# Kernel optimization log

Measured on AMD Instinct MI355X. Metric: run time of the kernel, lower is better.

The kernel has to match this reference:

```python
import jax, jax.numpy as jnp
import numpy as np

B, S, HID = 1, 2048, 4096
H, KH, D = 32, 8, 128          # query heads, kv heads, head_dim
ROT = 64                       # rotary_dim = head_dim * partial_rotary_factor (0.5)
THETA = 10000.0
EPS = 1e-5
SCALE = D ** -0.5
NEG = -1e30


def setup_inputs() -> dict:
    key = jax.random.key(0)
    ks = jax.random.split(key, 7)
    return {
        "hidden_states": jax.random.normal(ks[0], (B, S, HID), jnp.float32),
        "Wq": jax.random.normal(ks[1], (H * D, HID), jnp.float32) * 0.02,
        "Wk": jax.random.normal(ks[2], (KH * D, HID), jnp.float32) * 0.02,
        "Wv": jax.random.normal(ks[3], (KH * D, HID), jnp.float32) * 0.02,
        "Wo": jax.random.normal(ks[4], (H * D, HID), jnp.float32).T.reshape(HID, H * D) * 0.02,
        "q_norm_w": jax.random.uniform(ks[5], (D,), jnp.float32),
        "k_norm_w": jax.random.uniform(ks[6], (D,), jnp.float32),
        "position_ids": jnp.arange(S, dtype=jnp.int32)[None, :],
    }


def rms_norm(x, w):
    # per-head RMSNorm in fp32, scale by (weight + 1)
    xf = x.astype(jnp.float32)
    var = jnp.mean(xf * xf, axis=-1, keepdims=True)
    return (xf * jax.lax.rsqrt(var + EPS) * (w.astype(jnp.float32) + 1.0)).astype(x.dtype)


def rope_cos_sin(position_ids):
    inv_freq = 1.0 / (THETA ** (jnp.arange(0, ROT, 2, dtype=jnp.float32) / ROT))
    freqs = position_ids.astype(jnp.float32)[..., None] * inv_freq  # [B,S,ROT/2]
    emb = jnp.concatenate([freqs, freqs], axis=-1)                  # [B,S,ROT]
    return jnp.cos(emb)[:, None], jnp.sin(emb)[:, None]             # [B,1,S,ROT]


def rotate_half(x):
    x1, x2 = jnp.split(x, 2, axis=-1)
    return jnp.concatenate([-x2, x1], axis=-1)


def apply_partial_rope(x, cos, sin):
    x_rot, x_pass = x[..., :ROT], x[..., ROT:]
    x_rot = x_rot * cos + rotate_half(x_rot) * sin
    return jnp.concatenate([x_rot, x_pass], axis=-1)


def reference(hidden_states, Wq, Wk, Wv, Wo, q_norm_w, k_norm_w, position_ids):
    # projections -> [B, heads, S, D]
    q = (hidden_states @ Wq.T).reshape(B, S, H, D).transpose(0, 2, 1, 3)
    k = (hidden_states @ Wk.T).reshape(B, S, KH, D).transpose(0, 2, 1, 3)
    v = (hidden_states @ Wv.T).reshape(B, S, KH, D).transpose(0, 2, 1, 3)

    q = rms_norm(q, q_norm_w)
    k = rms_norm(k, k_norm_w)

    cos, sin = rope_cos_sin(position_ids)
    q = apply_partial_rope(q, cos, sin)
    k = apply_partial_rope(k, cos, sin)

    # repeat kv heads (GQA) -> [B, H, S, D]
    rep = H // KH
    k = jnp.broadcast_to(k[:, :, None], (B, KH, rep, S, D)).reshape(B, H, S, D)
    v = jnp.broadcast_to(v[:, :, None], (B, KH, rep, S, D)).reshape(B, H, S, D)

    scores = jnp.einsum("bhqd,bhkd->bhqk", q, k) * SCALE
    causal = jnp.tril(jnp.ones((S, S), bool))
    scores = jnp.where(causal, scores, NEG)
    attn = jax.nn.softmax(scores, axis=-1)
    out = jnp.einsum("bhqk,bhkd->bhqd", attn, v)        # [B,H,S,D]
    out = out.transpose(0, 2, 1, 3).reshape(B, S, H * D)
    return out @ Wo.T                                    # [B,S,HID]
```

## Files before the change

kernel.cpp:

```cpp
#include <hip/hip_runtime.h>
#include <hip/hip_bf16.h>

#define AS1 __attribute__((address_space(1)))
#define AS3 __attribute__((address_space(3)))

typedef __attribute__((ext_vector_type(8))) short short8;
typedef __attribute__((ext_vector_type(4))) short short4v;
typedef __attribute__((ext_vector_type(4))) float f32x4;

constexpr int S_ = 2048;
constexpr int HID_ = 4096;
constexpr int NH = 32;
constexpr int NKH = 8;
constexpr float EPS_ = 1e-5f;
constexpr float SCALE_ = 0.08838834764831845f;

__device__ __forceinline__ short f2bf(float f) {
  __hip_bfloat16 h = __float2bfloat16(f);
  return *reinterpret_cast<short*>(&h);
}

__global__ __launch_bounds__(256) void cast_bf16_kernel(const float4* __restrict__ src,
                                                        short4v* __restrict__ dst, int n4) {
  int i = blockIdx.x * 256 + threadIdx.x;
  if (i >= n4) return;
  float4 v = src[i];
  short4v o;
  o[0] = f2bf(v.x); o[1] = f2bf(v.y); o[2] = f2bf(v.z); o[3] = f2bf(v.w);
  dst[i] = o;
}

template <int G>
__global__ __launch_bounds__(512, 2) void gemm8_bt(const short* __restrict__ A,
                                                   const short* __restrict__ B,
                                                   float* __restrict__ C,
                                                   int M, int N, int K) {
  constexpr int BN = G * 64;
  constexpr int BUFSZ = 32768 + G * 8192;
  constexpr int GH = (G + 1) / 2;
  extern __shared__ __align__(16) char smem[];
  const int t = threadIdx.x, w = t >> 6, lane = t & 63;
  const int nbx = N / BN;
  int wg = blockIdx.x;
  const int cpx = gridDim.x >> 3;
  wg = (wg & 7) * cpx + (wg >> 3);
  const int by = wg / nbx, bx = wg % nbx;
  const long m0 = (long)by * 256, n0 = (long)bx * BN;
  const int wr = w >> 2, wc = w & 3;
  const int l15 = lane & 15, l4 = lane >> 4;
  const int NT = K >> 6;

  f32x4 acc[8][G];
#pragma unroll
  for (int f = 0; f < 8; ++f)
#pragma unroll
    for (int g = 0; g < G; ++g) acc[f][g] = (f32x4){0.f, 0.f, 0.f, 0.f};

  const int srow = w * 8 + (lane >> 3);
  const int schunk = lane & 7;

  auto STAGE = [&](int tile, int unit) {
    int tb = tile & (NT - 1);
    long k0 = (long)tb << 6;
    char* base = smem + (tb & 1) * BUFSZ;
    if (unit < 2) {
#pragma unroll
      for (int j = 0; j < 2; ++j) {
        int row = unit * 128 + j * 64 + srow;
        int ch = schunk ^ (row & 7);
        __builtin_amdgcn_global_load_lds(
            (const AS1 void*)(A + (m0 + row) * K + k0 + ch * 8),
            (AS3 void*)(base + unit * 16384 + j * 8192 + w * 1024 + lane * 16), 16, 0, 0);
      }
    } else {
      int bj = unit - 2;
      int row = bj * 64 + srow;
      int ch = schunk ^ (row & 7);
      __builtin_amdgcn_global_load_lds(
          (const AS1 void*)(B + (n0 + row) * K + k0 + ch * 8),
          (AS3 void*)(base + 32768 + bj * 8192 + w * 1024 + lane * 16), 16, 0, 0);
    }
  };
  auto LDA = [&](int buf, int f, int s) -> short8 {
    int ra = wr * 128 + f * 16 + l15;
    int byte = ra * 128 + (((s << 2) + l4) ^ (ra & 7)) * 16;
    return *(const short8*)(smem + buf * BUFSZ + byte);
  };
  auto LDB = [&](int buf, int g, int s) -> short8 {
    int rb = wc * (G * 16) + g * 16 + l15;
    int byte = 32768 + rb * 128 + (((s << 2) + l4) ^ (rb & 7)) * 16;
    return *(const short8*)(smem + buf * BUFSZ + byte);
  };

#pragma unroll
  for (int u = 0; u < 2 + G; ++u) STAGE(0, u);
  STAGE(1, 0);
  asm volatile("s_waitcnt vmcnt(2)" ::: "memory");
  asm volatile("s_barrier" ::: "memory");

  short8 af[4][2], bf2[G][2];
  for (int tt = 0; tt < NT; ++tt) {
    const int buf = tt & 1;
#pragma unroll
    for (int f = 0; f < 4; ++f) { af[f][0] = LDA(buf, f, 0); af[f][1] = LDA(buf, f, 1); }
#pragma unroll
    for (int g = 0; g < GH; ++g) { bf2[g][0] = LDB(buf, g, 0); bf2[g][1] = LDB(buf, g, 1); }
    STAGE(tt + 1, 1);
    asm volatile("s_barrier" ::: "memory");
    __builtin_amdgcn_s_setprio(1);
#pragma unroll
    for (int f = 0; f < 4; ++f)
#pragma unroll
      for (int g = 0; g < GH; ++g) {
        acc[f][g] = __builtin_amdgcn_mfma_f32_16x16x32_bf16(af[f][0], bf2[g][0], acc[f][g], 0, 0, 0);
        acc[f][g] = __builtin_amdgcn_mfma_f32_16x16x32_bf16(af[f][1], bf2[g][1], acc[f][g], 0, 0, 0);
      }
    __builtin_amdgcn_s_setprio(0);
    asm volatile("s_barrier" ::: "memory");
#pragma unroll
    for (int g = GH; g < G; ++g) { bf2[g][0] = LDB(buf, g, 0); bf2[g][1] = LDB(buf, g, 1); }
#pragma unroll
    for (int u = 2; u < G + 1; ++u) STAGE(tt + 1, u);
    asm volatile("s_barrier" ::: "memory");
    __builtin_amdgcn_s_setprio(1);
#pragma unroll
    for (int f = 0; f < 4; ++f)
#pragma unroll
      for (int g = GH; g < G; ++g) {
        acc[f][g] = __builtin_amdgcn_mfma_f32_16x16x32_bf16(af[f][0], bf2[g][0], acc[f][g], 0, 0, 0);
        acc[f][g] = __builtin_amdgcn_mfma_f32_16x16x32_bf16(af[f][1], bf2[g][1], acc[f][g], 0, 0, 0);
      }
    __builtin_amdgcn_s_setprio(0);
    asm volatile("s_barrier" ::: "memory");
#pragma unroll
    for (int f = 0; f < 4; ++f) { af[f][0] = LDA(buf, 4 + f, 0); af[f][1] = LDA(buf, 4 + f, 1); }
    STAGE(tt + 1, G + 1);
    asm volatile("s_barrier" ::: "memory");
    __builtin_amdgcn_s_setprio(1);
#pragma unroll
    for (int f = 0; f < 4; ++f)
#pragma unroll
      for (int g = 0; g < GH; ++g) {
        acc[4 + f][g] = __builtin_amdgcn_mfma_f32_16x16x32_bf16(af[f][0], bf2[g][0], acc[4 + f][g], 0, 0, 0);
        acc[4 + f][g] = __builtin_amdgcn_mfma_f32_16x16x32_bf16(af[f][1], bf2[g][1], acc[4 + f][g], 0, 0, 0);
      }
    __builtin_amdgcn_s_setprio(0);
    asm volatile("s_barrier" ::: "memory");
    STAGE(tt + 2, 0);
    asm volatile("s_barrier" ::: "memory");
    __builtin_amdgcn_s_setprio(1);
#pragma unroll
    for (int f = 0; f < 4; ++f)
#pragma unroll
      for (int g = GH; g < G; ++g) {
        acc[4 + f][g] = __builtin_amdgcn_mfma_f32_16x16x32_bf16(af[f][0], bf2[g][0], acc[4 + f][g], 0, 0, 0);
        acc[4 + f][g] = __builtin_amdgcn_mfma_f32_16x16x32_bf16(af[f][1], bf2[g][1], acc[4 + f][g], 0, 0, 0);
      }
    __builtin_amdgcn_s_setprio(0);
    asm volatile("s_waitcnt vmcnt(2)" ::: "memory");
    asm volatile("s_barrier" ::: "memory");
  }
#pragma unroll
  for (int f = 0; f < 8; ++f)
#pragma unroll
    for (int g = 0; g < G; ++g)
#pragma unroll
      for (int r = 0; r < 4; ++r) {
        long m = m0 + wr * 128 + f * 16 + l4 * 4 + r;
        long n = n0 + wc * (G * 16) + g * 16 + l15;
        C[m * N + n] = acc[f][g][r];
      }
}

__global__ __launch_bounds__(256) void normrope_kernel(const float* __restrict__ QKV,
    const int* __restrict__ pos_ids, const float* __restrict__ qw,
    const float* __restrict__ kw,
    short* __restrict__ Qn, short* __restrict__ Kn) {
  const int lane = threadIdx.x & 63;
  const long row = (long)blockIdx.x * 4 + (threadIdx.x >> 6);
  const long NQ = (long)S_ * NH;
  const float* src;
  short* dst;
  const float* wv;
  int s;
  float scl = 1.f;
  if (row < NQ) {
    s = (int)(row >> 5); int h = (int)(row & 31);
    src = QKV + (long)s * 6144 + h * 128;
    dst = Qn + ((long)h * S_ + s) * 128;
    wv = qw; scl = SCALE_;
  } else {
    long r2 = row - NQ; s = (int)(r2 >> 3); int kh = (int)(r2 & 7);
    src = QKV + (long)s * 6144 + 4096 + kh * 128;
    dst = Kn + ((long)kh * S_ + s) * 128;
    wv = kw;
  }
  float x0 = src[lane], x1 = src[lane + 64];
  float ss = x0 * x0 + x1 * x1;
#pragma unroll
  for (int m = 1; m < 64; m <<= 1) ss += __shfl_xor(ss, m);
  float inv = rsqrtf(ss * (1.f / 128.f) + EPS_);
  x0 = x0 * inv * (wv[lane] + 1.f);
  x1 = x1 * inv * (wv[lane + 64] + 1.f);
  int pos = pos_ids[s];
  int i = lane & 31;
  float invf = expf(-logf(10000.f) * ((float)(2 * i) / 64.f));
  float f = (float)pos * invf;
  float c = cosf(f), sn = sinf(f);
  float p = __shfl_xor(x0, 32);
  x0 = (lane < 32) ? (x0 * c - p * sn) : (x0 * c + p * sn);
  dst[lane] = f2bf(x0 * scl);
  dst[lane + 64] = f2bf(x1 * scl);
}

__global__ __launch_bounds__(256) void vtrans_kernel(const float* __restrict__ QKV,
                                                     short* __restrict__ Vt) {
  __shared__ __align__(16) float lt[64][68];
  const int t = threadIdx.x;
  const int s0 = blockIdx.x * 64, d0 = blockIdx.y * 64, kh = blockIdx.z;
  const float* src = QKV + (long)s0 * 6144 + 5120 + kh * 128 + d0;
#pragma unroll
  for (int i = 0; i < 4; ++i) {
    int idx = t + i * 256;
    int r = idx >> 4, c4 = (idx & 15) * 4;
    float4 v = *(const float4*)(src + (long)r * 6144 + c4);
    *(float4*)&lt[r][c4] = v;
  }
  __syncthreads();
  int d = t >> 2, seg = (t & 3) * 16;
  short* dst = Vt + ((long)kh * 128 + d0 + d) * S_ + s0 + seg;
  short8 a, b2;
#pragma unroll
  for (int j = 0; j < 8; ++j) a[j] = f2bf(lt[seg + j][d]);
#pragma unroll
  for (int j = 0; j < 8; ++j) b2[j] = f2bf(lt[seg + 8 + j][d]);
  *(short8*)dst = a;
  *(short8*)(dst + 8) = b2;
}

__global__ __launch_bounds__(512, 2) void attn_kernel(const short* __restrict__ Qn,
    const short* __restrict__ Kn, const short* __restrict__ Vt,
    short* __restrict__ O) {
  __shared__ __align__(16) short Ks[64 * 128];
  __shared__ __align__(16) short Vs[128 * 64];
  __shared__ __align__(16) short Ps[8][16 * 64];
  const int t = threadIdx.x, w = t >> 6, lane = t & 63;
  const int b = blockIdx.x;
  const int h = b & 31, qt = 15 - (b >> 5);
  const int kh = h >> 2;
  const int q0 = qt * 128;
  const int l15 = lane & 15, lk = (lane >> 4) * 8;

  short8 qf[4];
  {
    const short* Qh = Qn + ((long)h * S_ + q0 + w * 16) * 128;
#pragma unroll
    for (int ks = 0; ks < 4; ++ks)
      qf[ks] = *(const short8*)(Qh + l15 * 128 + ks * 32 + lk);
  }
  f32x4 o[8];
#pragma unroll
  for (int nf = 0; nf < 8; ++nf) o[nf] = (f32x4){0.f, 0.f, 0.f, 0.f};
  float mrun[4], lrun[4];
#pragma unroll
  for (int r = 0; r < 4; ++r) { mrun[r] = -1e30f; lrun[r] = 0.f; }

  const short* Khp = Kn + (long)kh * S_ * 128;
  const short* Vtp = Vt + (long)kh * 128 * S_;

  const int krr = w * 8 + (lane >> 4);
  const int kc = lane & 15;
  const int vdd = w * 16 + (lane >> 3);
  const int vc = lane & 7;
  char* pw = (char*)Ps[w];
  const int mrow = (lane >> 4) * 4;

  for (int kv0 = 0; kv0 < q0 + 128; kv0 += 64) {
#pragma unroll
    for (int j = 0; j < 2; ++j) {
      int rr = krr + j * 4;
      __builtin_amdgcn_global_load_lds(
          (const AS1 void*)(Khp + (long)(kv0 + rr) * 128 + ((kc ^ (rr & 7)) * 8)),
          (AS3 void*)(Ks + (w * 8 + j * 4) * 128 + lane * 8), 16, 0, 0);
    }
#pragma unroll
    for (int j = 0; j < 2; ++j) {
      int d = vdd + j * 8;
      __builtin_amdgcn_global_load_lds(
          (const AS1 void*)(Vtp + (long)d * S_ + kv0 + ((vc ^ (d & 7)) * 8)),
          (AS3 void*)(Vs + (w * 16 + j * 8) * 64 + lane * 8), 16, 0, 0);
    }
    __syncthreads();

    const bool active = (kv0 <= q0 + w * 16 + 15);
    if (active) {
      f32x4 sc[4];
#pragma unroll
      for (int ni = 0; ni < 4; ++ni) sc[ni] = (f32x4){0.f, 0.f, 0.f, 0.f};
#pragma unroll
      for (int ks = 0; ks < 4; ++ks)
#pragma unroll
        for (int ni = 0; ni < 4; ++ni) {
          int row = ni * 16 + l15;
          int bb = row * 256 + (ks * 32 + lk) * 2; bb ^= (row & 7) << 4;
          short8 kf = *(const short8*)((const char*)Ks + bb);
          sc[ni] = __builtin_amdgcn_mfma_f32_16x16x32_bf16(qf[ks], kf, sc[ni], 0, 0, 0);
        }
      if (kv0 + 64 > q0 + w * 16) {
#pragma unroll
        for (int ni = 0; ni < 4; ++ni)
#pragma unroll
          for (int r = 0; r < 4; ++r) {
            int qm = q0 + w * 16 + mrow + r;
            int kcol = kv0 + ni * 16 + l15;
            if (kcol > qm) sc[ni][r] = -1e30f;
          }
      }
      short pb[4][4];
#pragma unroll
      for (int r = 0; r < 4; ++r) {
        float mx = fmaxf(fmaxf(sc[0][r], sc[1][r]), fmaxf(sc[2][r], sc[3][r]));
        mx = fmaxf(mx, __shfl_xor(mx, 1));
        mx = fmaxf(mx, __shfl_xor(mx, 2));
        mx = fmaxf(mx, __shfl_xor(mx, 4));
        mx = fmaxf(mx, __shfl_xor(mx, 8));
        float mnew = fmaxf(mrun[r], mx);
        float scale = expf(mrun[r] - mnew);
        mrun[r] = mnew;
        float ssum = 0.f;
#pragma unroll
        for (int ni = 0; ni < 4; ++ni) {
          float p = expf(sc[ni][r] - mnew);
          ssum += p;
          pb[ni][r] = f2bf(p);
        }
        ssum += __shfl_xor(ssum, 1);
        ssum += __shfl_xor(ssum, 2);
        ssum += __shfl_xor(ssum, 4);
        ssum += __shfl_xor(ssum, 8);
        lrun[r] = lrun[r] * scale + ssum;
#pragma unroll
        for (int nf = 0; nf < 8; ++nf) o[nf][r] *= scale;
      }
#pragma unroll
      for (int ni = 0; ni < 4; ++ni)
#pragma unroll
        for (int r = 0; r < 4; ++r) {
          int m = mrow + r;
          int bb = m * 128 + (ni * 16 + l15) * 2; bb ^= (m & 7) << 4;
          *(short*)(pw + bb) = pb[ni][r];
        }
#pragma unroll
      for (int ks2 = 0; ks2 < 2; ++ks2) {
        int bp = l15 * 128 + (ks2 * 32 + lk) * 2; bp ^= (l15 & 7) << 4;
        short8 pf = *(const short8*)(pw + bp);
#pragma unroll
        for (int nf = 0; nf < 8; ++nf) {
          int bv = (nf * 16 + l15) * 128 + (ks2 * 32 + lk) * 2; bv ^= (l15 & 7) << 4;
          short8 vf = *(const short8*)((const char*)Vs + bv);
          o[nf] = __builtin_amdgcn_mfma_f32_16x16x32_bf16(pf, vf, o[nf], 0, 0, 0);
        }
      }
    }
    __syncthreads();
  }
#pragma unroll
  for (int r = 0; r < 4; ++r) {
    float invl = 1.f / lrun[r];
    int m = q0 + w * 16 + mrow + r;
#pragma unroll
    for (int nf = 0; nf < 8; ++nf)
      O[(long)m * 4096 + h * 128 + nf * 16 + l15] = f2bf(o[nf][r] * invl);
  }
}

extern "C" void kernel_launch(void* const* d_in, const int* in_sizes, int n_in,
                              void* d_out, int out_size, void* d_ws, size_t ws_size,
                              hipStream_t stream) {
  const float* hidden = (const float*)d_in[0];
  const float* Wq = (const float*)d_in[1];
  const float* Wk = (const float*)d_in[2];
  const float* Wv = (const float*)d_in[3];
  const float* Wo = (const float*)d_in[4];
  const float* qw = (const float*)d_in[5];
  const float* kw = (const float*)d_in[6];
  const int* pos = (const int*)d_in[7];
  float* out = (float*)d_out;

  char* ws = (char*)d_ws;
  short* hid_bf  = (short*)(ws + 0);
  short* Wqkv_bf = (short*)(ws + 16777216L);
  short* Wo_bf   = (short*)(ws + 67108864L);
  float* QKVf    = (float*)(ws + 100663296L);
  short* Qn      = (short*)(ws + 150994944L);
  short* Kn      = (short*)(ws + 167772160L);
  short* Vt      = (short*)(ws + 171966464L);
  short* AO      = hid_bf;

  (void)hipFuncSetAttribute((const void*)gemm8_bt<3>,
                            hipFuncAttributeMaxDynamicSharedMemorySize, 114688);
  (void)hipFuncSetAttribute((const void*)gemm8_bt<2>,
                            hipFuncAttributeMaxDynamicSharedMemorySize, 98304);

  auto cast = [&](const float* s_, short* d_, long n) {
    int n4 = (int)(n / 4);
    cast_bf16_kernel<<<(n4 + 255) / 256, 256, 0, stream>>>((const float4*)s_, (short4v*)d_, n4);
  };
  cast(hidden, hid_bf, (long)S_ * HID_);
  cast(Wq, Wqkv_bf, (long)4096 * 4096);
  cast(Wk, Wqkv_bf + (long)4096 * 4096, (long)1024 * 4096);
  cast(Wv, Wqkv_bf + (long)5120 * 4096, (long)1024 * 4096);
  cast(Wo, Wo_bf, (long)4096 * 4096);

  gemm8_bt<3><<<dim3(256), 512, 114688, stream>>>(hid_bf, Wqkv_bf, QKVf, S_, 6144, HID_);

  normrope_kernel<<<(S_ * (NH + NKH)) / 4, 256, 0, stream>>>(QKVf, pos, qw, kw, Qn, Kn);
  vtrans_kernel<<<dim3(S_ / 64, 2, NKH), 256, 0, stream>>>(QKVf, Vt);
  attn_kernel<<<dim3(512), 512, 0, stream>>>(Qn, Kn, Vt, AO);

  gemm8_bt<2><<<dim3(256), 512, 98304, stream>>>(AO, Wo_bf, out, S_, HID_, HID_);
}
```

Baseline: 524.4 us.

## Double-buffer attention KV tiles, widen per-wave Q rows, fuse casts, use exp2

The attention kernel now runs 4 waves that each own 32 query rows, which doubles K/V fragment reuse per wave. It double-buffers K/V tiles in dynamic LDS so the next tile's global-to-LDS load overlaps compute. The softmax scale is folded with log2(e) so exp2f can replace expf. The five cast launches are merged into one kernel, and the GEMM block-index decode is simplified. In exchange the kernel uses more LDS and registers, and the GEMM index change hardcodes 8 row blocks.

```diff
diff --git a/kernel.cpp b/kernel.cpp
--- a/kernel.cpp
+++ b/kernel.cpp
@@ -14,20 +14,32 @@
 constexpr int NKH = 8;
 constexpr float EPS_ = 1e-5f;
 constexpr float SCALE_ = 0.08838834764831845f;
+constexpr float SCL2E_ = 0.12751879524622712f;
 
 __device__ __forceinline__ short f2bf(float f) {
   __hip_bfloat16 h = __float2bfloat16(f);
   return *reinterpret_cast<short*>(&h);
 }
 
-__global__ __launch_bounds__(256) void cast_bf16_kernel(const float4* __restrict__ src,
-                                                        short4v* __restrict__ dst, int n4) {
-  int i = blockIdx.x * 256 + threadIdx.x;
-  if (i >= n4) return;
-  float4 v = src[i];
-  short4v o;
-  o[0] = f2bf(v.x); o[1] = f2bf(v.y); o[2] = f2bf(v.z); o[3] = f2bf(v.w);
-  dst[i] = o;
+__global__ __launch_bounds__(256) void cast_all_kernel(
+    const float4* __restrict__ h, const float4* __restrict__ wq,
+    const float4* __restrict__ wk, const float4* __restrict__ wv,
+    const float4* __restrict__ wo,
+    short4v* __restrict__ hd, short4v* __restrict__ wqkvd,
+    short4v* __restrict__ wod) {
+  long i = (long)blockIdx.x * 256 + threadIdx.x;
+  const float4* s;
+  short4v* d;
+  long o;
+  if (i < 2097152L)        { s = h;  d = hd;              o = i; }
+  else if (i < 6291456L)   { s = wq; d = wqkvd;           o = i - 2097152L; }
+  else if (i < 7340032L)   { s = wk; d = wqkvd + 4194304L; o = i - 6291456L; }
+  else if (i < 8388608L)   { s = wv; d = wqkvd + 5242880L; o = i - 7340032L; }
+  else                     { s = wo; d = wod;             o = i - 8388608L; }
+  float4 v = s[o];
+  short4v r;
+  r[0] = f2bf(v.x); r[1] = f2bf(v.y); r[2] = f2bf(v.z); r[3] = f2bf(v.w);
+  d[o] = r;
 }
 
 template <int G>
@@ -40,11 +52,10 @@
   constexpr int GH = (G + 1) / 2;
   extern __shared__ __align__(16) char smem[];
   const int t = threadIdx.x, w = t >> 6, lane = t & 63;
-  const int nbx = N / BN;
   int wg = blockIdx.x;
   const int cpx = gridDim.x >> 3;
   wg = (wg & 7) * cpx + (wg >> 3);
-  const int by = wg / nbx, bx = wg % nbx;
+  const int by = wg & 7, bx = wg >> 3;
   const long m0 = (long)by * 256, n0 = (long)bx * BN;
   const int wr = w >> 2, wc = w & 3;
   const int l15 = lane & 15, l4 = lane >> 4;
@@ -188,7 +199,7 @@
     s = (int)(row >> 5); int h = (int)(row & 31);
     src = QKV + (long)s * 6144 + h * 128;
     dst = Qn + ((long)h * S_ + s) * 128;
-    wv = qw; scl = SCALE_;
+    wv = qw; scl = SCL2E_;
   } else {
     long r2 = row - NQ; s = (int)(r2 >> 3); int kh = (int)(r2 & 7);
     src = QKV + (long)s * 6144 + 4096 + kh * 128;
@@ -238,140 +249,165 @@
   *(short8*)(dst + 8) = b2;
 }
 
-__global__ __launch_bounds__(512, 2) void attn_kernel(const short* __restrict__ Qn,
+__global__ __launch_bounds__(256, 2) void attn_kernel(const short* __restrict__ Qn,
     const short* __restrict__ Kn, const short* __restrict__ Vt,
     short* __restrict__ O) {
-  __shared__ __align__(16) short Ks[64 * 128];
-  __shared__ __align__(16) short Vs[128 * 64];
-  __shared__ __align__(16) short Ps[8][16 * 64];
+  extern __shared__ __align__(16) char smem[];
   const int t = threadIdx.x, w = t >> 6, lane = t & 63;
   const int b = blockIdx.x;
   const int h = b & 31, qt = 15 - (b >> 5);
   const int kh = h >> 2;
   const int q0 = qt * 128;
-  const int l15 = lane & 15, lk = (lane >> 4) * 8;
-
-  short8 qf[4];
+  const int l15 = lane & 15, l4 = lane >> 4, lk = l4 * 8;
+  const int mrow = l4 * 4;
+  char* pw = smem + 65536 + w * 4096;
+
+  short8 qf[2][4];
   {
-    const short* Qh = Qn + ((long)h * S_ + q0 + w * 16) * 128;
-#pragma unroll
-    for (int ks = 0; ks < 4; ++ks)
-      qf[ks] = *(const short8*)(Qh + l15 * 128 + ks * 32 + lk);
+    const short* Qh = Qn + ((long)h * S_ + q0 + w * 32) * 128;
+#pragma unroll
+    for (int mf = 0; mf < 2; ++mf)
+#pragma unroll
+      for (int ks = 0; ks < 4; ++ks)
+        qf[mf][ks] = *(const short8*)(Qh + (mf * 16 + l15) * 128 + ks * 32 + lk);
   }
-  f32x4 o[8];
-#pragma unroll
-  for (int nf = 0; nf < 8; ++nf) o[nf] = (f32x4){0.f, 0.f, 0.f, 0.f};
-  float mrun[4], lrun[4];
-#pragma unroll
-  for (int r = 0; r < 4; ++r) { mrun[r] = -1e30f; lrun[r] = 0.f; }
+  f32x4 o[2][8];
+#pragma unroll
+  for (int mf = 0; mf < 2; ++mf)
+#pragma unroll
+    for (int nf = 0; nf < 8; ++nf) o[mf][nf] = (f32x4){0.f, 0.f, 0.f, 0.f};
+  float mrun[2][4], lrun[2][4];
+#pragma unroll
+  for (int mf = 0; mf < 2; ++mf)
+#pragma unroll
+    for (int r = 0; r < 4; ++r) { mrun[mf][r] = -1e30f; lrun[mf][r] = 0.f; }
 
   const short* Khp = Kn + (long)kh * S_ * 128;
   const short* Vtp = Vt + (long)kh * 128 * S_;
-
-  const int krr = w * 8 + (lane >> 4);
-  const int kc = lane & 15;
-  const int vdd = w * 16 + (lane >> 3);
-  const int vc = lane & 7;
-  char* pw = (char*)Ps[w];
-  const int mrow = (lane >> 4) * 4;
-
-  for (int kv0 = 0; kv0 < q0 + 128; kv0 += 64) {
-#pragma unroll
-    for (int j = 0; j < 2; ++j) {
-      int rr = krr + j * 4;
+  const int NTIL = 2 * qt + 2;
+
+  auto STAGE = [&](int it) {
+    const int kv0 = it * 64;
+    char* kd = smem + (it & 1) * 16384;
+    char* vd = smem + 32768 + (it & 1) * 16384;
+#pragma unroll
+    for (int j = 0; j < 4; ++j) {
+      int row = (w * 4 + j) * 4 + l4;
+      int ch = l15 ^ (row & 7);
       __builtin_amdgcn_global_load_lds(
-          (const AS1 void*)(Khp + (long)(kv0 + rr) * 128 + ((kc ^ (rr & 7)) * 8)),
-          (AS3 void*)(Ks + (w * 8 + j * 4) * 128 + lane * 8), 16, 0, 0);
+          (const AS1 void*)(Khp + (long)(kv0 + row) * 128 + ch * 8),
+          (AS3 void*)(kd + (w * 4 + j) * 1024 + lane * 16), 16, 0, 0);
     }
 #pragma unroll
-    for (int j = 0; j < 2; ++j) {
-      int d = vdd + j * 8;
+    for (int j = 0; j < 4; ++j) {
+      int d = (w * 4 + j) * 8 + (lane >> 3);
+      int ch = (lane & 7) ^ (d & 7);
       __builtin_amdgcn_global_load_lds(
-          (const AS1 void*)(Vtp + (long)d * S_ + kv0 + ((vc ^ (d & 7)) * 8)),
-          (AS3 void*)(Vs + (w * 16 + j * 8) * 64 + lane * 8), 16, 0, 0);
+          (const AS1 void*)(Vtp + (long)d * S_ + kv0 + ch * 8),
+          (AS3 void*)(vd + (w * 4 + j) * 1024 + lane * 16), 16, 0, 0);
     }
-    __syncthreads();
-
-    const bool active = (kv0 <= q0 + w * 16 + 15);
-    if (active) {
-      f32x4 sc[4];
-#pragma unroll
-      for (int ni = 0; ni < 4; ++ni) sc[ni] = (f32x4){0.f, 0.f, 0.f, 0.f};
+  };
+
+  STAGE(0);
+  asm volatile("s_waitcnt vmcnt(0)" ::: "memory");
+  asm volatile("s_barrier" ::: "memory");
+
+  for (int it = 0; it < NTIL; ++it) {
+    const int kv0 = it * 64;
+    const char* kd = smem + (it & 1) * 16384;
+    const char* vd = smem + 32768 + (it & 1) * 16384;
+    if (it + 1 < NTIL) STAGE(it + 1);
+
+    if (kv0 < q0 + w * 32 + 32) {
+      f32x4 sc[2][4];
+#pragma unroll
+      for (int mf = 0; mf < 2; ++mf)
+#pragma unroll
+        for (int ni = 0; ni < 4; ++ni) sc[mf][ni] = (f32x4){0.f, 0.f, 0.f, 0.f};
 #pragma unroll
       for (int ks = 0; ks < 4; ++ks)
 #pragma unroll
         for (int ni = 0; ni < 4; ++ni) {
           int row = ni * 16 + l15;
-          int bb = row * 256 + (ks * 32 + lk) * 2; bb ^= (row & 7) << 4;
-          short8 kf = *(const short8*)((const char*)Ks + bb);
-          sc[ni] = __builtin_amdgcn_mfma_f32_16x16x32_bf16(qf[ks], kf, sc[ni], 0, 0, 0);
+          int bb = row * 256 + ((((ks << 2) + l4) ^ (row & 7)) << 4);
+          short8 kf = *(const short8*)(kd + bb);
+          sc[0][ni] = __builtin_amdgcn_mfma_f32_16x16x32_bf16(qf[0][ks], kf, sc[0][ni], 0, 0, 0);
+          sc[1][ni] = __builtin_amdgcn_mfma_f32_16x16x32_bf16(qf[1][ks], kf, sc[1][ni], 0, 0, 0);
         }
-      if (kv0 + 64 > q0 + w * 16) {
-#pragma unroll
-        for (int ni = 0; ni < 4; ++ni)
-#pragma unroll
-          for (int r = 0; r < 4; ++r) {
-            int qm = q0 + w * 16 + mrow + r;
-            int kcol = kv0 + ni * 16 + l15;
-            if (kcol > qm) sc[ni][r] = -1e30f;
+#pragma unroll
+      for (int mf = 0; mf < 2; ++mf)
+        if (kv0 + 64 > q0 + w * 32 + mf * 16) {
+#pragma unroll
+          for (int ni = 0; ni < 4; ++ni)
+#pragma unroll
+            for (int r = 0; r < 4; ++r) {
+              int qm = q0 + w * 32 + mf * 16 + mrow + r;
+              int kcol = kv0 + ni * 16 + l15;
+              if (kcol > qm) sc[mf][ni][r] = -1e30f;
+            }
+        }
+#pragma unroll
+      for (int mf = 0; mf < 2; ++mf)
+#pragma unroll
+        for (int r = 0; r < 4; ++r) {
+          float mx = fmaxf(fmaxf(sc[mf][0][r], sc[mf][1][r]), fmaxf(sc[mf][2][r], sc[mf][3][r]));
+          mx = fmaxf(mx, __shfl_xor(mx, 1));
+          mx = fmaxf(mx, __shfl_xor(mx, 2));
+          mx = fmaxf(mx, __shfl_xor(mx, 4));
+          mx = fmaxf(mx, __shfl_xor(mx, 8));
+          float mnew = fmaxf(mrun[mf][r], mx);
+          float scale = exp2f(mrun[mf][r] - mnew);
+          mrun[mf][r] = mnew;
+          float ssum = 0.f;
+          short pbv[4];
+#pragma unroll
+          for (int ni = 0; ni < 4; ++ni) {
+            float p = exp2f(sc[mf][ni][r] - mnew);
+            ssum += p;
+            pbv[ni] = f2bf(p);
           }
-      }
-      short pb[4][4];
-#pragma unroll
-      for (int r = 0; r < 4; ++r) {
-        float mx = fmaxf(fmaxf(sc[0][r], sc[1][r]), fmaxf(sc[2][r], sc[3][r]));
-        mx = fmaxf(mx, __shfl_xor(mx, 1));
-        mx = fmaxf(mx, __shfl_xor(mx, 2));
-        mx = fmaxf(mx, __shfl_xor(mx, 4));
-        mx = fmaxf(mx, __shfl_xor(mx, 8));
-        float mnew = fmaxf(mrun[r], mx);
-        float scale = expf(mrun[r] - mnew);
-        mrun[r] = mnew;
-        float ssum = 0.f;
-#pragma unroll
-        for (int ni = 0; ni < 4; ++ni) {
-          float p = expf(sc[ni][r] - mnew);
-          ssum += p;
-          pb[ni][r] = f2bf(p);
+          ssum += __shfl_xor(ssum, 1);
+          ssum += __shfl_xor(ssum, 2);
+          ssum += __shfl_xor(ssum, 4);
+          ssum += __shfl_xor(ssum, 8);
+          lrun[mf][r] = lrun[mf][r] * scale + ssum;
+#pragma unroll
+          for (int nf = 0; nf < 8; ++nf) o[mf][nf][r] *= scale;
+          int m = mf * 16 + mrow + r;
+#pragma unroll
+          for (int ni = 0; ni < 4; ++ni) {
+            int bb = (m * 128 + (ni * 16 + l15) * 2) ^ ((m & 7) << 4);
+            *(short*)(pw + bb) = pbv[ni];
+          }
         }
-        ssum += __shfl_xor(ssum, 1);
-        ssum += __shfl_xor(ssum, 2);
-        ssum += __shfl_xor(ssum, 4);
-        ssum += __shfl_xor(ssum, 8);
-        lrun[r] = lrun[r] * scale + ssum;
-#pragma unroll
-        for (int nf = 0; nf < 8; ++nf) o[nf][r] *= scale;
-      }
-#pragma unroll
-      for (int ni = 0; ni < 4; ++ni)
-#pragma unroll
-        for (int r = 0; r < 4; ++r) {
-          int m = mrow + r;
-          int bb = m * 128 + (ni * 16 + l15) * 2; bb ^= (m & 7) << 4;
-          *(short*)(pw + bb) = pb[ni][r];
+#pragma unroll
+      for (int ks2 = 0; ks2 < 2; ++ks2) {
+        int rq0 = l15, rq1 = 16 + l15;
+        short8 pf0 = *(const short8*)(pw + ((rq0 * 128 + (ks2 * 32 + lk) * 2) ^ ((rq0 & 7) << 4)));
+        short8 pf1 = *(const short8*)(pw + ((rq1 * 128 + (ks2 * 32 + lk) * 2) ^ ((rq1 & 7) << 4)));
+#pragma unroll
+        for (int nf = 0; nf < 8; ++nf) {
+          int d = nf * 16 + l15;
+          int bv = d * 128 + ((((ks2 << 2) + l4) ^ (d & 7)) << 4);
+          short8 vf = *(const short8*)(vd + bv);
+          o[0][nf] = __builtin_amdgcn_mfma_f32_16x16x32_bf16(pf0, vf, o[0][nf], 0, 0, 0);
+          o[1][nf] = __builtin_amdgcn_mfma_f32_16x16x32_bf16(pf1, vf, o[1][nf], 0, 0, 0);
         }
-#pragma unroll
-      for (int ks2 = 0; ks2 < 2; ++ks2) {
-        int bp = l15 * 128 + (ks2 * 32 + lk) * 2; bp ^= (l15 & 7) << 4;
-        short8 pf = *(const short8*)(pw + bp);
-#pragma unroll
-        for (int nf = 0; nf < 8; ++nf) {
-          int bv = (nf * 16 + l15) * 128 + (ks2 * 32 + lk) * 2; bv ^= (l15 & 7) << 4;
-          short8 vf = *(const short8*)((const char*)Vs + bv);
-          o[nf] = __builtin_amdgcn_mfma_f32_16x16x32_bf16(pf, vf, o[nf], 0, 0, 0);
-        }
       }
     }
-    __syncthreads();
+    asm volatile("s_waitcnt vmcnt(0)" ::: "memory");
+    asm volatile("s_barrier" ::: "memory");
   }
 #pragma unroll
-  for (int r = 0; r < 4; ++r) {
-    float invl = 1.f / lrun[r];
-    int m = q0 + w * 16 + mrow + r;
-#pragma unroll
-    for (int nf = 0; nf < 8; ++nf)
-      O[(long)m * 4096 + h * 128 + nf * 16 + l15] = f2bf(o[nf][r] * invl);
-  }
+  for (int mf = 0; mf < 2; ++mf)
+#pragma unroll
+    for (int r = 0; r < 4; ++r) {
+      float invl = 1.f / lrun[mf][r];
+      int m = q0 + w * 32 + mf * 16 + mrow + r;
+#pragma unroll
+      for (int nf = 0; nf < 8; ++nf)
+        O[(long)m * 4096 + h * 128 + nf * 16 + l15] = f2bf(o[mf][nf][r] * invl);
+    }
 }
 
 extern "C" void kernel_launch(void* const* d_in, const int* in_sizes, int n_in,
@@ -401,22 +437,20 @@
                             hipFuncAttributeMaxDynamicSharedMemorySize, 114688);
   (void)hipFuncSetAttribute((const void*)gemm8_bt<2>,
                             hipFuncAttributeMaxDynamicSharedMemorySize, 98304);
-
-  auto cast = [&](const float* s_, short* d_, long n) {
-    int n4 = (int)(n / 4);
-    cast_bf16_kernel<<<(n4 + 255) / 256, 256, 0, stream>>>((const float4*)s_, (short4v*)d_, n4);
-  };
-  cast(hidden, hid_bf, (long)S_ * HID_);
-  cast(Wq, Wqkv_bf, (long)4096 * 4096);
-  cast(Wk, Wqkv_bf + (long)4096 * 4096, (long)1024 * 4096);
-  cast(Wv, Wqkv_bf + (long)5120 * 4096, (long)1024 * 4096);
-  cast(Wo, Wo_bf, (long)4096 * 4096);
+  (void)hipFuncSetAttribute((const void*)attn_kernel,
+                            hipFuncAttributeMaxDynamicSharedMemorySize, 81920);
+
+  cast_all_kernel<<<49152, 256, 0, stream>>>(
+      (const float4*)hidden, (const float4*)Wq, (const float4*)Wk,
+      (const float4*)Wv, (const float4*)Wo,
+      (short4v*)hid_bf, (short4v*)Wqkv_bf, (short4v*)Wo_bf);
 
   gemm8_bt<3><<<dim3(256), 512, 114688, stream>>>(hid_bf, Wqkv_bf, QKVf, S_, 6144, HID_);
 
   normrope_kernel<<<(S_ * (NH + NKH)) / 4, 256, 0, stream>>>(QKVf, pos, qw, kw, Qn, Kn);
   vtrans_kernel<<<dim3(S_ / 64, 2, NKH), 256, 0, stream>>>(QKVf, Vt);
-  attn_kernel<<<dim3(512), 512, 0, stream>>>(Qn, Kn, Vt, AO);
+
+  attn_kernel<<<dim3(512), 256, 81920, stream>>>(Qn, Kn, Vt, AO);
 
   gemm8_bt<2><<<dim3(256), 512, 98304, stream>>>(AO, Wo_bf, out, S_, HID_, HID_);
 }
```

Result: no change. 533.4 us (+1.7%).
